# Optimization experiments

Measured on AMD Instinct MI355X. Metric: run time of the kernel, lower is better.

## Reference

```python
import jax, jax.numpy as jnp
import numpy as np

NJ, ND, NQ, NC, NAV = 4, 32, 32, 64, 2
N = 131072

def silu(x):
    return x * jax.nn.sigmoid(x)

def conv1d(x, w, b, stride=1):
    # x: [n, Cin, L], w: [Cout, Cin, K] (torch OIH layout)
    y = jax.lax.conv_general_dilated(x, w, (stride,), 'VALID',
                                     dimension_numbers=('NCH', 'OIH', 'NCH'))
    return y + b[None, :, None]

def dijet_cat(x, d):
    # x: [n, nd, 12], d: [n, nd, 6] -> interleave pairs of x with d -> [n, nd, 18]
    n, nd, _ = x.shape
    return jnp.concatenate([x.reshape(n, nd, 6, 2), d[..., None]], axis=3).reshape(n, nd, 18)

def quad_cat(x, q):
    # x: [n, nq, 6], q: [n, nq, 3] -> [n, nq, 9]
    n, nq, _ = x.shape
    return jnp.concatenate([x.reshape(n, nq, 3, 2), q[..., None]], axis=3).reshape(n, nq, 9)

def rotate(p, R):
    return p.at[:, 2, :].set(((p[:, 2, :] + 1.0 + R) % 2.0) - 1.0)

def flip_phi(p):
    return p.at[:, 2, :].multiply(-1.0)

def flip_eta(p):
    return p.at[:, 1, :].multiply(-1.0)

def inv_part(p, da, qa, W_td, b_td, W_db, b_db, W_dr1, b_dr1, W_dr2, b_dr2,
             W_tq, b_tq, W_qb, b_qb, W_qr1, b_qr1, W_qr2, b_qr2):
    p = conv1d(p, W_td, b_td)                 # [n, nd, 12]
    d = conv1d(p, W_db, b_db, stride=2)       # [n, nd-2, 6]
    d = jnp.concatenate([d, da], axis=1)      # [n, nd, 6]
    d0 = d
    d = silu(d)
    d = conv1d(dijet_cat(p, d), W_dr1, b_dr1, stride=3) + d0
    d = silu(d)
    d = conv1d(dijet_cat(p, d), W_dr2, b_dr2, stride=3) + d0
    d = silu(d)
    d = conv1d(d, W_tq, b_tq)                 # [n, nq, 6]
    q = conv1d(d, W_qb, b_qb, stride=2)       # [n, nq-2, 3]
    q = jnp.concatenate([q, qa], axis=1)      # [n, nq, 3]
    q0 = q
    q = silu(q)
    q = conv1d(quad_cat(d, q), W_qr1, b_qr1, stride=3) + q0
    q = silu(q)
    q = conv1d(quad_cat(d, q), W_qr2, b_qr2, stride=3) + q0
    return silu(q)                            # [n, nq, 3]

def setup_inputs() -> dict:
    key = jax.random.key(0)
    ks = jax.random.split(key, 24)
    s = 0.1
    inp = {
        'x': jax.random.normal(ks[0], (N, NJ, 12), jnp.float32),
        'p': jax.random.normal(ks[1], (N, NJ, 12), jnp.float32),
        'da': jax.random.normal(ks[2], (N, 12), jnp.float32),
        'qa': jax.random.normal(ks[3], (N, 6), jnp.float32),
        'va': jax.random.normal(ks[4], (N, NAV), jnp.float32),
        'W_td': jax.random.normal(ks[5], (ND, NJ, 1), jnp.float32) * s,
        'b_td': jax.random.normal(ks[6], (ND,), jnp.float32) * s,
        'W_db': jax.random.normal(ks[7], (ND - 2, ND, 2), jnp.float32) * s,
        'b_db': jax.random.normal(ks[8], (ND - 2,), jnp.float32) * s,
        'W_dr1': jax.random.normal(ks[9], (ND, ND, 3), jnp.float32) * s,
        'b_dr1': jax.random.normal(ks[10], (ND,), jnp.float32) * s,
        'W_dr2': jax.random.normal(ks[11], (ND, ND, 3), jnp.float32) * s,
        'b_dr2': jax.random.normal(ks[12], (ND,), jnp.float32) * s,
        'W_tq': jax.random.normal(ks[13], (NQ, ND, 1), jnp.float32) * s,
        'b_tq': jax.random.normal(ks[14], (NQ,), jnp.float32) * s,
        'W_qb': jax.random.normal(ks[15], (NQ - 2, NQ, 2), jnp.float32) * s,
        'b_qb': jax.random.normal(ks[16], (NQ - 2,), jnp.float32) * s,
        'W_qr1': jax.random.normal(ks[17], (NQ, NQ, 3), jnp.float32) * s,
        'b_qr1': jax.random.normal(ks[18], (NQ,), jnp.float32) * s,
        'W_qr2': jax.random.normal(ks[19], (NQ, NQ, 3), jnp.float32) * s,
        'b_qr2': jax.random.normal(ks[20], (NQ,), jnp.float32) * s,
        'W_tv': jax.random.normal(ks[21], (NC, NQ + NAV, 1), jnp.float32) * s,
        'b_tv': jax.random.normal(ks[22], (NC,), jnp.float32) * s,
        'W_v1': jax.random.normal(jax.random.fold_in(key, 101), (NC, NC, 1), jnp.float32) * s,
        'b_v1': jax.random.normal(jax.random.fold_in(key, 102), (NC,), jnp.float32) * s,
        'W_v2': jax.random.normal(jax.random.fold_in(key, 103), (NC, NC, 1), jnp.float32) * s,
        'b_v2': jax.random.normal(jax.random.fold_in(key, 104), (NC,), jnp.float32) * s,
        'W_vs': jax.random.normal(jax.random.fold_in(key, 105), (1, NC, 3), jnp.float32) * s,
        'b_vs': jax.random.normal(jax.random.fold_in(key, 106), (1,), jnp.float32) * s,
    }
    return inp

def reference(x, p, da, qa, va,
              W_td, b_td, W_db, b_db, W_dr1, b_dr1, W_dr2, b_dr2,
              W_tq, b_tq, W_qb, b_qb, W_qr1, b_qr1, W_qr2, b_qr2,
              W_tv, b_tv, W_v1, b_v1, W_v2, b_v2, W_vs, b_vs):
    n = p.shape[0]
    da2 = da.reshape(n, 2, 6)
    qa2 = qa.reshape(n, 2, 3)
    va3 = jnp.broadcast_to(va[:, :NAV, None], (n, NAV, 3))
    params = (W_td, b_td, W_db, b_db, W_dr1, b_dr1, W_dr2, b_dr2,
              W_tq, b_tq, W_qb, b_qb, W_qr1, b_qr1, W_qr2, b_qr2)
    # eval mode: nR=1, R=[0], randomR=0; 4-fold phi/eta flip symmetrization
    p0 = rotate(p, 0.0)
    p1 = flip_phi(p0)
    p2 = flip_eta(p1)
    p3 = flip_eta(p0)
    q = (inv_part(p0, da2, qa2, *params) + inv_part(p1, da2, qa2, *params)
         + inv_part(p2, da2, qa2, *params) + inv_part(p3, da2, qa2, *params)) / 4.0
    v = jnp.concatenate([q, va3], axis=1)     # [n, nq+nAv, 3]
    v = conv1d(v, W_tv, b_tv)                 # [n, nc, 3]
    v0 = v
    v = silu(v)
    v = conv1d(v, W_v1, b_v1) + v0
    v = silu(v)
    v = conv1d(v, W_v2, b_v2) + v0
    v = silu(v)
    v = conv1d(v, W_vs, b_vs)                 # [n, 1, 1]
    return v.reshape(n, -1)
```

## Files before the change

### kernel.cpp

```cpp
#include <hip/hip_runtime.h>


typedef _Float16 f16x8 __attribute__((ext_vector_type(8)));
typedef float f32x4 __attribute__((ext_vector_type(4)));
typedef __fp16 fp16x2 __attribute__((ext_vector_type(2)));

#define TILES 50
#define WS_BIAS    12800
#define NBIAS      416
#define QSUM_DW    13216

#define CIN(k) (16*(((k)>>2)&1) + 4*((k)>>3) + ((k)&3))

__device__ __forceinline__ float silu_f(float x){
    return x * __builtin_amdgcn_rcpf(1.0f + __expf(-x));
}
__device__ __forceinline__ f32x4 silu4(f32x4 v){
    f32x4 r; r.x=silu_f(v.x); r.y=silu_f(v.y); r.z=silu_f(v.z); r.w=silu_f(v.w);
    return r;
}
__device__ __forceinline__ unsigned pk(float a, float b){
    fp16x2 h = __builtin_amdgcn_cvt_pkrtz(a, b);
    return __builtin_bit_cast(unsigned, h);
}
#define PACKB(RES, T0, T1) {                                                   \
    (RES).x = pk((T0).x,(T0).y); (RES).y = pk((T0).z,(T0).w);                  \
    (RES).z = pk((T1).x,(T1).y); (RES).w = pk((T1).z,(T1).w); }


__device__ float l1_Ad0(const float* Wdb, const float* Wtd, int c, int k){
    int h = k>>2, jr = k&3; float a = 0.f;
    for (int i=0;i<32;++i) a += Wdb[64*c+2*i+h]*Wtd[4*i+jr];
    return a;
}
__device__ float l1_AB(const float* Wdb,const float* bdb,const float* btd,int c){
    float b = bdb[c];
    for (int i=0;i<32;++i) b += (Wdb[64*c+2*i]+Wdb[64*c+2*i+1])*btd[i];
    return b;
}
__device__ float l1_M(const float* Wdr,const float* Wtd,int c,int k){
    int h=k>>2, jr=k&3; float a=0.f;
    for(int i=0;i<32;++i) a += Wdr[96*c+3*i+h]*Wtd[4*i+jr];
    return a;
}
__device__ float l1_MB(const float* Wdr,const float* bdr,const float* btd,int c){
    float b = bdr[c];
    for(int i=0;i<32;++i) b += (Wdr[96*c+3*i]+Wdr[96*c+3*i+1])*btd[i];
    return b;
}
__device__ float qn_Q(const float* Wqb, const float* Wtq, int c, int kg){
    int z=kg>>5, kk=kg&31; float a=0.f;
    for(int i=0;i<32;++i) a += Wqb[64*c+2*i+z]*Wtq[32*i+kk];
    return a;
}
__device__ float qn_N(const float* Wqr, const float* Wtq, int c, int kg){
    int z=kg>>5, kk=kg&31; float a=0.f;
    for(int i=0;i<32;++i) a += Wqr[96*c+3*i+z]*Wtq[32*i+kk];
    return a;
}

__global__ void precompute(
    const float* __restrict__ Wtd, const float* __restrict__ btd,
    const float* __restrict__ Wdb, const float* __restrict__ bdb,
    const float* __restrict__ Wdr1, const float* __restrict__ bdr1,
    const float* __restrict__ Wdr2, const float* __restrict__ bdr2,
    const float* __restrict__ Wtq, const float* __restrict__ btq,
    const float* __restrict__ Wqb, const float* __restrict__ bqb,
    const float* __restrict__ Wqr1, const float* __restrict__ bqr1,
    const float* __restrict__ Wqr2, const float* __restrict__ bqr2,
    const float* __restrict__ Wtv, const float* __restrict__ btv,
    const float* __restrict__ Wv1, const float* __restrict__ bv1,
    const float* __restrict__ Wv2, const float* __restrict__ bv2,
    const float* __restrict__ Wvs,
    float* __restrict__ wsf)
{
    const int tid = blockIdx.x*blockDim.x + threadIdx.x;
    const int stride = gridDim.x*blockDim.x;

    for (int it = tid; it < TILES*64; it += stride) {
        const int tile = it >> 6, lane = it & 63;
        const int m = lane & 15, g = lane >> 4;
        float v[8];
        #pragma unroll
        for (int j = 0; j < 8; ++j) {
            const int k = 8*g + j;
            float val = 0.f;
            if (tile < 6) {
                const int r = 16*tile + m;
                if (r < 32) {
                    if (r < 30) {
                        if (k < 8)      val = l1_Ad0(Wdb, Wtd, r, k);
                        else if (k==8)  val = l1_AB(Wdb, bdb, btd, r);
                    } else if (r == 30) val = (k==9)  ? 1.f : 0.f;
                    else                val = (k==10) ? 1.f : 0.f;
                } else {
                    const float* Wdr = (r<64)? Wdr1 : Wdr2;
                    const float* bdr = (r<64)? bdr1 : bdr2;
                    const int c = (r<64)? r-32 : r-64;
                    if (k < 8) {
                        val = l1_M(Wdr, Wtd, c, k);
                        if (c < 30) val += l1_Ad0(Wdb, Wtd, c, k);
                    } else if (k == 8) {
                        val = l1_MB(Wdr, bdr, btd, c);
                        if (c < 30) val += l1_AB(Wdb, bdb, btd, c);
                    } else if (k == 9)  val = (c==30)? 1.f : 0.f;
                    else if (k == 10)   val = (c==31)? 1.f : 0.f;
                }
            } else if (tile < 8)  { val = Wdr1[96*(16*(tile-6)+m) + 3*CIN(k) + 2]; }
            else if (tile < 10)   { val = Wdr2[96*(16*(tile-8)+m) + 3*CIN(k) + 2]; }
            else if (tile < 22) {
                const int tt = tile-10, r = 16*(tt>>1)+m, kg = 32*(tt&1)+CIN(k);
                if (r < 32) { if (r < 30) val = qn_Q(Wqb, Wtq, r, kg); }
                else {
                    const float* Wqr = (r<64)? Wqr1 : Wqr2;
                    const int c = (r<64)? r-32 : r-64;
                    val = qn_N(Wqr, Wtq, c, kg);
                    if (c < 30) val += qn_Q(Wqb, Wtq, c, kg);
                }
            }
            else if (tile < 24)  { val = Wqr1[96*(16*(tile-22)+m) + 3*CIN(k) + 2]; }
            else if (tile < 26)  { val = Wqr2[96*(16*(tile-24)+m) + 3*CIN(k) + 2]; }
            else if (tile < 34) {
                const int tt = tile-26, r = 16*(tt>>1)+m;
                if ((tt&1)==0) val = 0.25f*Wtv[34*r + CIN(k)];
                else {
                    if (k==0) val = btv[r];
                    else if (k==1) val = Wtv[34*r+32];
                    else if (k==2) val = Wtv[34*r+33];
                }
            }
            else if (tile < 42) { const int tt=tile-34; val = Wv1[64*(16*(tt>>1)+m) + 32*(tt&1) + CIN(k)]; }
            else                { const int tt=tile-42; val = Wv2[64*(16*(tt>>1)+m) + 32*(tt&1) + CIN(k)]; }
            v[j] = val;
        }
        unsigned* wd = (unsigned*)wsf;
        const int base = tile*256 + lane*4;
        wd[base+0] = pk(v[0],v[1]);
        wd[base+1] = pk(v[2],v[3]);
        wd[base+2] = pk(v[4],v[5]);
        wd[base+3] = pk(v[6],v[7]);
    }

    for (int r = tid; r < NBIAS; r += stride) {
        float val = 0.f;
        if (r < 96) {
            if (r < 30) {
                float b = bqb[r];
                for (int i=0;i<32;++i) b += (Wqb[64*r+2*i]+Wqb[64*r+2*i+1])*btq[i];
                val = b;
            } else if (r >= 32) {
                const float* Wqr = (r<64)? Wqr1 : Wqr2;
                const float* bqr = (r<64)? bqr1 : bqr2;
                const int c = (r<64)? r-32 : r-64;
                float b = bqr[c];
                for (int i=0;i<32;++i) b += (Wqr[96*c+3*i]+Wqr[96*c+3*i+1])*btq[i];
                if (c < 30) {
                    float qb = bqb[c];
                    for (int i=0;i<32;++i) qb += (Wqb[64*c+2*i]+Wqb[64*c+2*i+1])*btq[i];
                    b += qb;
                }
                val = b;
            }
        }
        else if (r < 160) val = bv1[r-96];
        else if (r < 224) val = bv2[r-160];
        else { const int idx = r-224, lq = idx>>6, row = idx&63; val = Wvs[3*row + lq]; }
        wsf[WS_BIAS + r] = val;
    }
}


__global__ __launch_bounds__(256, 2) void resnet_part1(
    const float* __restrict__ P,  const float* __restrict__ DA,
    const float* __restrict__ QA, const float* __restrict__ wsf,
    unsigned* __restrict__ qsum, int n_total)
{
    __shared__ uint4 lw[26*64];
    __shared__ alignas(16) float fbA[96];

    {
        const uint4* src = (const uint4*)wsf;
        for (int i = threadIdx.x; i < 26*64; i += blockDim.x) lw[i] = src[i];
        uint4* fb4 = (uint4*)fbA;
        for (int i = threadIdx.x; i < 24; i += blockDim.x) fb4[i] = src[3200 + i];
    }
    __syncthreads();

    const int l  = threadIdx.x & 63;
    const int wv = threadIdx.x >> 6;
    const int c  = l & 15, g = l >> 4;
    const int s  = blockIdx.x*64 + wv*16 + c;
    const int sl = (s < n_total) ? s : (n_total-1);
    const bool g0 = (g==0), g1 = (g==1);

    const uint4* lwl = lw + l;
    #define LDA(T) __builtin_bit_cast(f16x8, lwl[(T)*64])
    #define MFMA(A,B,C) __builtin_amdgcn_mfma_f32_16x16x32_f16((A), __builtin_bit_cast(f16x8,(B)), (C), 0, 0, 0)

    const unsigned me = g0 ? 0x80000000u : 0u;
    const unsigned mp = g0 ? 0x00008000u : 0u;

    const f32x4 z4 = {0.f,0.f,0.f,0.f};

    #pragma unroll 1
    for (int lq = 0; lq < 3; ++lq) {
        uint4 xb[2];
        #pragma unroll
        for (int t = 0; t < 2; ++t) {
            const int pos = 4*lq + 2*t;
            float f0 = P[48*sl + pos],        f1 = P[48*sl + 12 + pos];
            float y0 = P[48*sl + 24 + pos] + 1.0f; y0 -= 2.0f*floorf(y0*0.5f);
            float f2 = y0 - 1.0f,             f3 = P[48*sl + 36 + pos];
            float f4 = P[48*sl + pos + 1],    f5 = P[48*sl + 12 + pos + 1];
            float y1 = P[48*sl + 24 + pos + 1] + 1.0f; y1 -= 2.0f*floorf(y1*0.5f);
            float f6 = y1 - 1.0f,             f7 = P[48*sl + 36 + pos + 1];
            float da0 = DA[12*sl + 2*lq + t];
            float da1 = DA[12*sl + 6 + 2*lq + t];
            uint4 xv; xv.x=0; xv.y=0; xv.z=0; xv.w=0;
            if (g0)      { xv.x = pk(f0,f1); xv.y = pk(f2,f3); xv.z = pk(f4,f5); xv.w = pk(f6,f7); }
            else if (g1) { xv.x = pk(1.0f, da0); xv.y = pk(da1, 0.0f); }
            xb[t] = xv;
        }
        const float qa30m = (g==3) ? QA[6*sl + lq]     : 0.0f;
        const float qa31m = (g==3) ? QA[6*sl + 3 + lq] : 0.0f;

        f32x4 qav0 = z4, qav1 = z4;

        #pragma unroll 1
        for (int var = 0; var < 4; ++var) {
            const unsigned fe = (var>=2)? me : 0u;
            const unsigned fp = (var==1||var==2)? mp : 0u;

            uint4 Bs[2];
            #pragma unroll
            for (int t = 0; t < 2; ++t) {
                uint4 Bxi;
                Bxi.x = xb[t].x ^ fe; Bxi.y = xb[t].y ^ fp;
                Bxi.z = xb[t].z ^ fe; Bxi.w = xb[t].w ^ fp;

                f32x4 a0 = MFMA(LDA(0), Bxi, z4);
                f32x4 a1 = MFMA(LDA(1), Bxi, z4);
                f32x4 a2 = MFMA(LDA(2), Bxi, z4);
                f32x4 a3 = MFMA(LDA(3), Bxi, z4);
                f32x4 a4 = MFMA(LDA(4), Bxi, z4);
                f32x4 a5 = MFMA(LDA(5), Bxi, z4);

                uint4 Bt;
                { f32x4 s0=silu4(a0), s1=silu4(a1); PACKB(Bt, s0, s1); }
                a2 = MFMA(LDA(6), Bt, a2);
                a3 = MFMA(LDA(7), Bt, a3);
                { f32x4 s0=silu4(a2), s1=silu4(a3); PACKB(Bt, s0, s1); }
                a4 = MFMA(LDA(8), Bt, a4);
                a5 = MFMA(LDA(9), Bt, a5);
                { f32x4 s0=silu4(a4), s1=silu4(a5); PACKB(Bs[t], s0, s1); }
            }

            f32x4 q[6];
            #pragma unroll
            for (int mt=0; mt<6; ++mt) {
                f32x4 acc = MFMA(LDA(10+2*mt), Bs[0], *(const f32x4*)&fbA[16*mt + 4*g]);
                q[mt] = MFMA(LDA(10+2*mt+1), Bs[1], acc);
            }
            q[1].z += qa30m; q[1].w += qa31m;
            q[3].z += qa30m; q[3].w += qa31m;
            q[5].z += qa30m; q[5].w += qa31m;

            uint4 Bq;
            { f32x4 s0=silu4(q[0]), s1=silu4(q[1]); PACKB(Bq, s0, s1); }
            q[2] = MFMA(LDA(22), Bq, q[2]);
            q[3] = MFMA(LDA(23), Bq, q[3]);
            { f32x4 s0=silu4(q[2]), s1=silu4(q[3]); PACKB(Bq, s0, s1); }
            q[4] = MFMA(LDA(24), Bq, q[4]);
            q[5] = MFMA(LDA(25), Bq, q[5]);
            qav0 += silu4(q[4]);
            qav1 += silu4(q[5]);
        }

        if (s < n_total) {
            const int rec = (lq*n_total + sl)*16;
            uint4 w0; PACKB(w0, qav0, qav1);
            *(uint4*)&qsum[rec + 4*g] = w0;
        }
    }
}


__global__ __launch_bounds__(256, 3) void resnet_part2(
    const float* __restrict__ VA, const float* __restrict__ wsf,
    const unsigned* __restrict__ qsum, const float* __restrict__ bvs,
    float* __restrict__ out, int n_total)
{
    __shared__ uint4 lw2[24*64];
    __shared__ alignas(16) float fbB[320];

    {
        const uint4* src = (const uint4*)wsf;
        for (int i = threadIdx.x; i < 24*64; i += blockDim.x) lw2[i] = src[26*64 + i];
        uint4* fb4 = (uint4*)fbB;
        for (int i = threadIdx.x; i < 80; i += blockDim.x) fb4[i] = src[3224 + i];
    }
    __syncthreads();

    const int l  = threadIdx.x & 63;
    const int wv = threadIdx.x >> 6;
    const int c  = l & 15, g = l >> 4;
    const int s  = blockIdx.x*64 + wv*16 + c;
    const int sl = (s < n_total) ? s : (n_total-1);
    const bool g0 = (g==0);

    const uint4* lwl = lw2 + l;
    #define LDB(T) __builtin_bit_cast(f16x8, lwl[((T)-26)*64])

    uint4 Bva; Bva.x=0; Bva.y=0; Bva.z=0; Bva.w=0;
    if (g0) {
        const float va0 = VA[2*sl], va1 = VA[2*sl+1];
        Bva.x = pk(1.0f, va0); Bva.y = pk(va1, 0.0f);
    }

    const f32x4 z4 = {0.f,0.f,0.f,0.f};
    float out_acc = 0.0f;

    #pragma unroll 1
    for (int lq = 0; lq < 3; ++lq) {
        const uint4 BQ = *(const uint4*)&qsum[(lq*n_total + sl)*16 + 4*g];

        f32x4 uacc[4], w[4];
        #pragma unroll
        for (int mt=0; mt<4; ++mt) {
            f32x4 acc = MFMA(LDB(26+2*mt), BQ, z4);
            uacc[mt] = MFMA(LDB(27+2*mt), Bva, acc);
        }
        uint4 B0, B1;
        { f32x4 t0=silu4(uacc[0]), t1=silu4(uacc[1]); PACKB(B0, t0, t1); }
        { f32x4 t0=silu4(uacc[2]), t1=silu4(uacc[3]); PACKB(B1, t0, t1); }
        #pragma unroll
        for (int mt=0; mt<4; ++mt) {
            f32x4 acc = MFMA(LDB(34+2*mt), B0, uacc[mt]);
            acc = MFMA(LDB(35+2*mt), B1, acc);
            w[mt] = acc + *(const f32x4*)&fbB[16*mt + 4*g];
        }
        { f32x4 t0=silu4(w[0]), t1=silu4(w[1]); PACKB(B0, t0, t1); }
        { f32x4 t0=silu4(w[2]), t1=silu4(w[3]); PACKB(B1, t0, t1); }
        #pragma unroll
        for (int mt=0; mt<4; ++mt) {
            f32x4 acc = MFMA(LDB(42+2*mt), B0, uacc[mt]);
            acc = MFMA(LDB(43+2*mt), B1, acc);
            w[mt] = acc + *(const f32x4*)&fbB[64 + 16*mt + 4*g];
        }
        #pragma unroll
        for (int mt=0; mt<4; ++mt) {
            const f32x4 wvs = *(const f32x4*)&fbB[128 + 64*lq + 16*mt + 4*g];
            out_acc += wvs.x*silu_f(w[mt].x) + wvs.y*silu_f(w[mt].y)
                     + wvs.z*silu_f(w[mt].z) + wvs.w*silu_f(w[mt].w);
        }
    }

    out_acc += __shfl_xor(out_acc, 16, 64);
    out_acc += __shfl_xor(out_acc, 32, 64);
    if (g == 0 && s < n_total) out[s] = out_acc + bvs[0];
}

extern "C" void kernel_launch(void* const* d_in, const int* in_sizes, int n_in,
                              void* d_out, int out_size, void* d_ws, size_t ws_size,
                              hipStream_t stream)
{
    (void)n_in; (void)ws_size; (void)out_size;
    const float* P   = (const float*)d_in[1];
    const float* DA  = (const float*)d_in[2];
    const float* QA  = (const float*)d_in[3];
    const float* VA  = (const float*)d_in[4];
    const float* Wtd = (const float*)d_in[5];   const float* btd = (const float*)d_in[6];
    const float* Wdb = (const float*)d_in[7];   const float* bdb = (const float*)d_in[8];
    const float* Wdr1= (const float*)d_in[9];   const float* bdr1= (const float*)d_in[10];
    const float* Wdr2= (const float*)d_in[11];  const float* bdr2= (const float*)d_in[12];
    const float* Wtq = (const float*)d_in[13];  const float* btq = (const float*)d_in[14];
    const float* Wqb = (const float*)d_in[15];  const float* bqb = (const float*)d_in[16];
    const float* Wqr1= (const float*)d_in[17];  const float* bqr1= (const float*)d_in[18];
    const float* Wqr2= (const float*)d_in[19];  const float* bqr2= (const float*)d_in[20];
    const float* Wtv = (const float*)d_in[21];  const float* btv = (const float*)d_in[22];
    const float* Wv1 = (const float*)d_in[23];  const float* bv1 = (const float*)d_in[24];
    const float* Wv2 = (const float*)d_in[25];  const float* bv2 = (const float*)d_in[26];
    const float* Wvs = (const float*)d_in[27];  const float* bvs = (const float*)d_in[28];
    float* out = (float*)d_out;

    const int n_total = in_sizes[1] / 48;
    float* wsf = (float*)d_ws;
    unsigned* qsum = (unsigned*)(wsf + QSUM_DW);

    precompute<<<dim3(64), dim3(256), 0, stream>>>(
        Wtd, btd, Wdb, bdb, Wdr1, bdr1, Wdr2, bdr2,
        Wtq, btq, Wqb, bqb, Wqr1, bqr1, Wqr2, bqr2,
        Wtv, btv, Wv1, bv1, Wv2, bv2, Wvs, wsf);

    const int grid = (n_total + 63) / 64;
    resnet_part1<<<dim3(grid), dim3(256), 0, stream>>>(
        P, DA, QA, wsf, qsum, n_total);
    resnet_part2<<<dim3(grid), dim3(256), 0, stream>>>(
        VA, wsf, qsum, bvs, out, n_total);
}
```

Before: 214.1 us.

## Fuse the two resnet kernels and keep quad sums in registers

Merges the invariant-part kernel and the final resnet kernel into a single kernel. The per-sample quad sums are packed to fp16 and fed straight into the second stage's MFMAs instead of being written to and read back from a global workspace buffer. This removes one kernel launch and the global round trip for the intermediate. In exchange the fused kernel holds all 50 weight tiles in LDS and has higher register pressure, which may lower occupancy or cause spills under the 2-block launch bound.

```diff
diff --git a/kernel.cpp b/kernel.cpp
--- a/kernel.cpp
+++ b/kernel.cpp
@@ -8,7 +8,6 @@
 #define TILES 50
 #define WS_BIAS    12800
 #define NBIAS      416
-#define QSUM_DW    13216
 
 #define CIN(k) (16*(((k)>>2)&1) + 4*((k)>>3) + ((k)&3))
 
@@ -170,19 +169,20 @@
 }
 
 
-__global__ __launch_bounds__(256, 2) void resnet_part1(
+__global__ __launch_bounds__(256, 2) void resnet_fused(
     const float* __restrict__ P,  const float* __restrict__ DA,
-    const float* __restrict__ QA, const float* __restrict__ wsf,
-    unsigned* __restrict__ qsum, int n_total)
+    const float* __restrict__ QA, const float* __restrict__ VA,
+    const float* __restrict__ wsf, const float* __restrict__ bvs,
+    float* __restrict__ out, int n_total)
 {
-    __shared__ uint4 lw[26*64];
-    __shared__ alignas(16) float fbA[96];
+    __shared__ uint4 lw[TILES*64];
+    __shared__ alignas(16) float fb[NBIAS];
 
     {
         const uint4* src = (const uint4*)wsf;
-        for (int i = threadIdx.x; i < 26*64; i += blockDim.x) lw[i] = src[i];
-        uint4* fb4 = (uint4*)fbA;
-        for (int i = threadIdx.x; i < 24; i += blockDim.x) fb4[i] = src[3200 + i];
+        for (int i = threadIdx.x; i < TILES*64; i += blockDim.x) lw[i] = src[i];
+        uint4* fb4 = (uint4*)fb;
+        for (int i = threadIdx.x; i < NBIAS/4; i += blockDim.x) fb4[i] = src[3200 + i];
     }
     __syncthreads();
 
@@ -200,7 +200,14 @@
     const unsigned me = g0 ? 0x80000000u : 0u;
     const unsigned mp = g0 ? 0x00008000u : 0u;
 
+    uint4 Bva; Bva.x=0; Bva.y=0; Bva.z=0; Bva.w=0;
+    if (g0) {
+        const float va0 = VA[2*sl], va1 = VA[2*sl+1];
+        Bva.x = pk(1.0f, va0); Bva.y = pk(va1, 0.0f);
+    }
+
     const f32x4 z4 = {0.f,0.f,0.f,0.f};
+    float out_acc = 0.0f;
 
     #pragma unroll 1
     for (int lq = 0; lq < 3; ++lq) {
@@ -258,7 +265,7 @@
             f32x4 q[6];
             #pragma unroll
             for (int mt=0; mt<6; ++mt) {
-                f32x4 acc = MFMA(LDA(10+2*mt), Bs[0], *(const f32x4*)&fbA[16*mt + 4*g]);
+                f32x4 acc = MFMA(LDA(10+2*mt), Bs[0], *(const f32x4*)&fb[16*mt + 4*g]);
                 q[mt] = MFMA(LDA(10+2*mt+1), Bs[1], acc);
             }
             q[1].z += qa30m; q[1].w += qa31m;
@@ -276,80 +283,33 @@
             qav1 += silu4(q[5]);
         }
 
-        if (s < n_total) {
-            const int rec = (lq*n_total + sl)*16;
-            uint4 w0; PACKB(w0, qav0, qav1);
-            *(uint4*)&qsum[rec + 4*g] = w0;
-        }
-    }
-}
-
-
-__global__ __launch_bounds__(256, 3) void resnet_part2(
-    const float* __restrict__ VA, const float* __restrict__ wsf,
-    const unsigned* __restrict__ qsum, const float* __restrict__ bvs,
-    float* __restrict__ out, int n_total)
-{
-    __shared__ uint4 lw2[24*64];
-    __shared__ alignas(16) float fbB[320];
-
-    {
-        const uint4* src = (const uint4*)wsf;
-        for (int i = threadIdx.x; i < 24*64; i += blockDim.x) lw2[i] = src[26*64 + i];
-        uint4* fb4 = (uint4*)fbB;
-        for (int i = threadIdx.x; i < 80; i += blockDim.x) fb4[i] = src[3224 + i];
-    }
-    __syncthreads();
-
-    const int l  = threadIdx.x & 63;
-    const int wv = threadIdx.x >> 6;
-    const int c  = l & 15, g = l >> 4;
-    const int s  = blockIdx.x*64 + wv*16 + c;
-    const int sl = (s < n_total) ? s : (n_total-1);
-    const bool g0 = (g==0);
-
-    const uint4* lwl = lw2 + l;
-    #define LDB(T) __builtin_bit_cast(f16x8, lwl[((T)-26)*64])
-
-    uint4 Bva; Bva.x=0; Bva.y=0; Bva.z=0; Bva.w=0;
-    if (g0) {
-        const float va0 = VA[2*sl], va1 = VA[2*sl+1];
-        Bva.x = pk(1.0f, va0); Bva.y = pk(va1, 0.0f);
-    }
-
-    const f32x4 z4 = {0.f,0.f,0.f,0.f};
-    float out_acc = 0.0f;
-
-    #pragma unroll 1
-    for (int lq = 0; lq < 3; ++lq) {
-        const uint4 BQ = *(const uint4*)&qsum[(lq*n_total + sl)*16 + 4*g];
-
+        uint4 BQ; PACKB(BQ, qav0, qav1);
         f32x4 uacc[4], w[4];
         #pragma unroll
         for (int mt=0; mt<4; ++mt) {
-            f32x4 acc = MFMA(LDB(26+2*mt), BQ, z4);
-            uacc[mt] = MFMA(LDB(27+2*mt), Bva, acc);
+            f32x4 acc = MFMA(LDA(26+2*mt), BQ, z4);
+            uacc[mt] = MFMA(LDA(27+2*mt), Bva, acc);
         }
         uint4 B0, B1;
         { f32x4 t0=silu4(uacc[0]), t1=silu4(uacc[1]); PACKB(B0, t0, t1); }
         { f32x4 t0=silu4(uacc[2]), t1=silu4(uacc[3]); PACKB(B1, t0, t1); }
         #pragma unroll
         for (int mt=0; mt<4; ++mt) {
-            f32x4 acc = MFMA(LDB(34+2*mt), B0, uacc[mt]);
-            acc = MFMA(LDB(35+2*mt), B1, acc);
-            w[mt] = acc + *(const f32x4*)&fbB[16*mt + 4*g];
+            f32x4 acc = MFMA(LDA(34+2*mt), B0, uacc[mt]);
+            acc = MFMA(LDA(35+2*mt), B1, acc);
+            w[mt] = acc + *(const f32x4*)&fb[96 + 16*mt + 4*g];
         }
         { f32x4 t0=silu4(w[0]), t1=silu4(w[1]); PACKB(B0, t0, t1); }
         { f32x4 t0=silu4(w[2]), t1=silu4(w[3]); PACKB(B1, t0, t1); }
         #pragma unroll
         for (int mt=0; mt<4; ++mt) {
-            f32x4 acc = MFMA(LDB(42+2*mt), B0, uacc[mt]);
-            acc = MFMA(LDB(43+2*mt), B1, acc);
-            w[mt] = acc + *(const f32x4*)&fbB[64 + 16*mt + 4*g];
+            f32x4 acc = MFMA(LDA(42+2*mt), B0, uacc[mt]);
+            acc = MFMA(LDA(43+2*mt), B1, acc);
+            w[mt] = acc + *(const f32x4*)&fb[160 + 16*mt + 4*g];
         }
         #pragma unroll
         for (int mt=0; mt<4; ++mt) {
-            const f32x4 wvs = *(const f32x4*)&fbB[128 + 64*lq + 16*mt + 4*g];
+            const f32x4 wvs = *(const f32x4*)&fb[224 + 64*lq + 16*mt + 4*g];
             out_acc += wvs.x*silu_f(w[mt].x) + wvs.y*silu_f(w[mt].y)
                      + wvs.z*silu_f(w[mt].z) + wvs.w*silu_f(w[mt].w);
         }
@@ -385,7 +345,6 @@
 
     const int n_total = in_sizes[1] / 48;
     float* wsf = (float*)d_ws;
-    unsigned* qsum = (unsigned*)(wsf + QSUM_DW);
 
     precompute<<<dim3(64), dim3(256), 0, stream>>>(
         Wtd, btd, Wdb, bdb, Wdr1, bdr1, Wdr2, bdr2,
@@ -393,8 +352,6 @@
         Wtv, btv, Wv1, bv1, Wv2, bv2, Wvs, wsf);
 
     const int grid = (n_total + 63) / 64;
-    resnet_part1<<<dim3(grid), dim3(256), 0, stream>>>(
-        P, DA, QA, wsf, qsum, n_total);
-    resnet_part2<<<dim3(grid), dim3(256), 0, stream>>>(
-        VA, wsf, qsum, bvs, out, n_total);
-}
+    resnet_fused<<<dim3(grid), dim3(256), 0, stream>>>(
+        P, DA, QA, VA, wsf, bvs, out, n_total);
+}
```

After: 252.0 us. 17.7% more time.
